# Performance work log

Hardware: AMD Instinct MI355X
Metric: run time of the kernel (lower is better)

## Reference

```python
import jax, jax.numpy as jnp
import numpy as np

D_MODEL = 1024
N_HEADS = 16
D_K = D_MODEL // N_HEADS
B, S = 2, 2048


def setup_inputs() -> dict:
    key = jax.random.key(0)
    ks = jax.random.split(key, 12)
    scale = 1.0 / np.sqrt(D_MODEL)
    inp = {
        "query": jax.random.normal(ks[0], (B, S, D_MODEL), jnp.float32),
        "key": jax.random.normal(ks[1], (B, S, D_MODEL), jnp.float32),
        "value": jax.random.normal(ks[2], (B, S, D_MODEL), jnp.float32),
        "mask": jnp.tril(jnp.ones((S, S), dtype=bool))[None, None],  # (1,1,S,S) causal
        "W_q": jax.random.normal(ks[3], (D_MODEL, D_MODEL), jnp.float32) * scale,
        "b_q": jnp.zeros((D_MODEL,), jnp.float32),
        "W_k": jax.random.normal(ks[4], (D_MODEL, D_MODEL), jnp.float32) * scale,
        "b_k": jnp.zeros((D_MODEL,), jnp.float32),
        "W_v": jax.random.normal(ks[5], (D_MODEL, D_MODEL), jnp.float32) * scale,
        "b_v": jnp.zeros((D_MODEL,), jnp.float32),
        "W_o": jax.random.normal(ks[6], (D_MODEL, D_MODEL), jnp.float32) * scale,
        "b_o": jnp.zeros((D_MODEL,), jnp.float32),
    }
    return inp


def reference(query, key, value, mask, W_q, b_q, W_k, b_k, W_v, b_v, W_o, b_o):
    b = query.shape[0]
    # Linear projections (torch Linear: x @ W.T + b), split into heads -> (b,h,s,d_k)
    def proj(x, W, bias):
        y = x @ W.T + bias
        return y.reshape(b, -1, N_HEADS, D_K).transpose(0, 2, 1, 3)

    q = proj(query, W_q, b_q)
    k = proj(key, W_k, b_k)
    v = proj(value, W_v, b_v)

    # scores: (b,h,sq,sk)
    scores = jnp.einsum("bhqd,bhkd->bhqk", q, k) / jnp.sqrt(jnp.float32(D_K)).astype(q.dtype)
    scores = jnp.where(mask, scores, jnp.finfo(scores.dtype).min)
    attn = jax.nn.softmax(scores, axis=-1)
    out = jnp.einsum("bhqk,bhkd->bhqd", attn, v)  # (b,h,sq,d_k)
    out = out.transpose(0, 2, 1, 3).reshape(b, -1, D_MODEL)
    return out @ W_o.T + b_o
```

## Files before the change

kernel.cpp:

```cpp
#include <hip/hip_runtime.h>
#include <hip/hip_bf16.h>
#include <stdint.h>

#define D_MODEL 1024
#define NH 16
#define DK 64
#define BB 2
#define SS 2048
#define MROWS (BB*SS)

typedef __attribute__((ext_vector_type(8))) short bf16x8;
typedef __attribute__((ext_vector_type(4))) float f32x4;

__device__ __forceinline__ short to_bf16(float f) {
  __hip_bfloat16 h = __float2bfloat16(f);
  union { __hip_bfloat16 b; short s; } u; u.b = h; return u.s;
}

__device__ __forceinline__ f32x4 mfma16(bf16x8 a, bf16x8 b, f32x4 c) {
  return __builtin_amdgcn_mfma_f32_16x16x32_bf16(a, b, c, 0, 0, 0);
}

__device__ __forceinline__ void gload_lds16(const void* g, void* l) {
  __builtin_amdgcn_global_load_lds(
      (const __attribute__((address_space(1))) unsigned int*)g,
      (__attribute__((address_space(3))) unsigned int*)l,
      16, 0, 0);
}

__global__ __launch_bounds__(256) void cvt3(const float* __restrict__ a,
                                            const float* __restrict__ b,
                                            const float* __restrict__ c,
                                            short* __restrict__ oa,
                                            short* __restrict__ ob,
                                            short* __restrict__ oc) {
  const int z = blockIdx.z;
  const float* x = z == 0 ? a : z == 1 ? b : c;
  short* y = z == 0 ? oa : z == 1 ? ob : oc;
  const int i = (blockIdx.x * 256 + threadIdx.x) * 4;
  const float4 v = *(const float4*)(x + i);
  short4 o;
  o.x = to_bf16(v.x); o.y = to_bf16(v.y); o.z = to_bf16(v.z); o.w = to_bf16(v.w);
  *(short4*)(y + i) = o;
}

__global__ __launch_bounds__(256) void cvt4(const float* __restrict__ a,
                                            const float* __restrict__ b,
                                            const float* __restrict__ c,
                                            const float* __restrict__ d,
                                            short* __restrict__ oa,
                                            short* __restrict__ ob,
                                            short* __restrict__ oc,
                                            short* __restrict__ od) {
  const int z = blockIdx.z;
  const float* x = z == 0 ? a : z == 1 ? b : z == 2 ? c : d;
  short* y = z == 0 ? oa : z == 1 ? ob : z == 2 ? oc : od;
  const int i = (blockIdx.x * 256 + threadIdx.x) * 4;
  const float4 v = *(const float4*)(x + i);
  short4 o;
  o.x = to_bf16(v.x); o.y = to_bf16(v.y); o.z = to_bf16(v.z); o.w = to_bf16(v.w);
  *(short4*)(y + i) = o;
}

__global__ __launch_bounds__(256) void gemm_qkv(const short* __restrict__ Xq,
                                                const short* __restrict__ Xk,
                                                const short* __restrict__ Xv,
                                                const short* __restrict__ Wq,
                                                const short* __restrict__ Wk,
                                                const short* __restrict__ Wv,
                                                const float* __restrict__ bq,
                                                const float* __restrict__ bk,
                                                const float* __restrict__ bv,
                                                short* __restrict__ Qh,
                                                short* __restrict__ Kh,
                                                short* __restrict__ VT) {
  constexpr int K = 1024;
  __shared__ short As[128 * 64];
  __shared__ short Bs[128 * 64];
  const int z = blockIdx.z;
  const short* A    = z == 0 ? Xq : z == 1 ? Xk : Xv;
  const short* Wt   = z == 0 ? Wq : z == 1 ? Wk : Wv;
  const float* bias = z == 0 ? bq : z == 1 ? bk : bv;

  const int tid = threadIdx.x;
  const int w = tid >> 6, lane = tid & 63;
  const int m0 = blockIdx.x * 128, n0 = blockIdx.y * 128;
  const int wm = w >> 1, wn = w & 1;
  const int fr = lane & 15, fg = lane >> 4;
  const int srow = tid >> 3, scol = (tid & 7) * 8;

  f32x4 acc[4][4] = {};

  for (int k0 = 0; k0 < K; k0 += 64) {
    __syncthreads();
#pragma unroll
    for (int i = 0; i < 4; ++i) {
      const int row = i * 32 + srow;
      gload_lds16(A  + (size_t)(m0 + row) * K + k0 + scol, As + row * 64 + scol);
      gload_lds16(Wt + (size_t)(n0 + row) * K + k0 + scol, Bs + row * 64 + scol);
    }
    asm volatile("s_waitcnt vmcnt(0)" ::: "memory");
    __syncthreads();

    bf16x8 af[4][2], bfr[4][2];
#pragma unroll
    for (int i = 0; i < 4; ++i)
#pragma unroll
      for (int hh = 0; hh < 2; ++hh) {
        af[i][hh]  = *(const bf16x8*)(As + (wm * 64 + i * 16 + fr) * 64 + hh * 32 + fg * 8);
        bfr[i][hh] = *(const bf16x8*)(Bs + (wn * 64 + i * 16 + fr) * 64 + hh * 32 + fg * 8);
      }
    __builtin_amdgcn_s_setprio(1);
#pragma unroll
    for (int mi = 0; mi < 4; ++mi)
#pragma unroll
      for (int ni = 0; ni < 4; ++ni) {
        acc[mi][ni] = mfma16(af[mi][0], bfr[ni][0], acc[mi][ni]);
        acc[mi][ni] = mfma16(af[mi][1], bfr[ni][1], acc[mi][ni]);
      }
    __builtin_amdgcn_s_setprio(0);
  }

  const float scale = (z == 0) ? 0.18033688011112042f : 1.0f;
#pragma unroll
  for (int mi = 0; mi < 4; ++mi)
#pragma unroll
    for (int ni = 0; ni < 4; ++ni) {
      const int col = n0 + wn * 64 + ni * 16 + fr;
      const float bval = bias[col];
      const int h = col >> 6, d = col & 63;
#pragma unroll
      for (int r = 0; r < 4; ++r) {
        const int row = m0 + wm * 64 + mi * 16 + fg * 4 + r;
        const float val = (acc[mi][ni][r] + bval) * scale;
        const int b = row >> 11, s = row & (SS - 1);
        if (z < 2) {
          short* dst = (z == 0) ? Qh : Kh;
          dst[((size_t)(b * NH + h) * SS + s) * DK + d] = to_bf16(val);
        } else {
          VT[((size_t)(b * NH + h) * DK + d) * SS + s] = to_bf16(val);
        }
      }
    }
}

__global__ __launch_bounds__(256) void gemm_out(const short* __restrict__ A,
                                                const short* __restrict__ Wt,
                                                const float* __restrict__ bias,
                                                float* __restrict__ Y) {
  constexpr int K = 1024;
  __shared__ short As[128 * 64];
  __shared__ short Bs[64 * 64];
  const int tid = threadIdx.x;
  const int w = tid >> 6, lane = tid & 63;
  const int m0 = blockIdx.x * 128, n0 = blockIdx.y * 64;
  const int wm = w >> 1, wn = w & 1;
  const int fr = lane & 15, fg = lane >> 4;
  const int srow = tid >> 3, scol = (tid & 7) * 8;

  f32x4 acc[4][2] = {};

  for (int k0 = 0; k0 < K; k0 += 64) {
    __syncthreads();
#pragma unroll
    for (int i = 0; i < 4; ++i) {
      const int row = i * 32 + srow;
      gload_lds16(A + (size_t)(m0 + row) * K + k0 + scol, As + row * 64 + scol);
    }
#pragma unroll
    for (int i = 0; i < 2; ++i) {
      const int row = i * 32 + srow;
      gload_lds16(Wt + (size_t)(n0 + row) * K + k0 + scol, Bs + row * 64 + scol);
    }
    asm volatile("s_waitcnt vmcnt(0)" ::: "memory");
    __syncthreads();

    bf16x8 af[4][2], bfr[2][2];
#pragma unroll
    for (int i = 0; i < 4; ++i)
#pragma unroll
      for (int hh = 0; hh < 2; ++hh)
        af[i][hh] = *(const bf16x8*)(As + (wm * 64 + i * 16 + fr) * 64 + hh * 32 + fg * 8);
#pragma unroll
    for (int i = 0; i < 2; ++i)
#pragma unroll
      for (int hh = 0; hh < 2; ++hh)
        bfr[i][hh] = *(const bf16x8*)(Bs + (wn * 32 + i * 16 + fr) * 64 + hh * 32 + fg * 8);
    __builtin_amdgcn_s_setprio(1);
#pragma unroll
    for (int mi = 0; mi < 4; ++mi)
#pragma unroll
      for (int ni = 0; ni < 2; ++ni) {
        acc[mi][ni] = mfma16(af[mi][0], bfr[ni][0], acc[mi][ni]);
        acc[mi][ni] = mfma16(af[mi][1], bfr[ni][1], acc[mi][ni]);
      }
    __builtin_amdgcn_s_setprio(0);
  }

#pragma unroll
  for (int mi = 0; mi < 4; ++mi)
#pragma unroll
    for (int ni = 0; ni < 2; ++ni) {
      const int col = n0 + wn * 32 + ni * 16 + fr;
      const float bval = bias[col];
#pragma unroll
      for (int r = 0; r < 4; ++r) {
        const int row = m0 + wm * 64 + mi * 16 + fg * 4 + r;
        Y[(size_t)row * D_MODEL + col] = acc[mi][ni][r] + bval;
      }
    }
}

__global__ __launch_bounds__(256, 2) void attn_kernel(const short* __restrict__ Qh,
                                                      const short* __restrict__ Kh,
                                                      const short* __restrict__ VT,
                                                      short* __restrict__ AO) {
  __shared__ short P_lds[4][2][16 * 64];
  const int tid = threadIdx.x, w = tid >> 6, lane = tid & 63;
  const int fr = lane & 15, fg = lane >> 4;
  const int kr = fg * 4;

  const int bid = blockIdx.x;
  const int lid = ((bid & 7) << 6) | (bid >> 3);
  const int bh = lid >> 4;
  const int xq = lid & 15;
  const int b = bh >> 4, h = bh & 15;

  const int strip = (w == 0) ? xq : (w == 1) ? (31 - xq) : (w == 2) ? (32 + xq) : (63 - xq);
  const int q0w = strip * 32;

  const short* Qp = Qh + (size_t)bh * SS * DK;
  const short* Kp = Kh + (size_t)bh * SS * DK;
  const short* Vp = VT + (size_t)bh * DK * SS;

  bf16x8 qf[2][2];
#pragma unroll
  for (int qt = 0; qt < 2; ++qt)
#pragma unroll
    for (int hh = 0; hh < 2; ++hh)
      qf[qt][hh] = *(const bf16x8*)(Qp + (size_t)(q0w + qt * 16 + fr) * DK + hh * 32 + fg * 8);

  const short onev = (fr == 0) ? (short)0x3F80 : (short)0;
  const bf16x8 af4 = {onev, onev, onev, onev, onev, onev, onev, onev};

  f32x4 o[5][2] = {};
  float m_run[2] = {-1e30f, -1e30f};

  const int nfull = q0w >> 6;
  const int swz = (fr & 7) << 4;

  bf16x8 kf[4][2];
#pragma unroll
  for (int kt = 0; kt < 4; ++kt)
#pragma unroll
    for (int hh = 0; hh < 2; ++hh)
      kf[kt][hh] = *(const bf16x8*)(Kp + (size_t)(kt * 16 + fr) * DK + hh * 32 + fg * 8);

  for (int ti = 0; ti <= nfull; ++ti) {
    const int k0 = ti * 64;
    const bool hasNext = ti < nfull;

    bf16x8 kn[4][2];
    if (hasNext) {
#pragma unroll
      for (int kt = 0; kt < 4; ++kt)
#pragma unroll
        for (int hh = 0; hh < 2; ++hh)
          kn[kt][hh] = *(const bf16x8*)(Kp + (size_t)(k0 + 64 + kt * 16 + fr) * DK + hh * 32 + fg * 8);
    }

    f32x4 st[4][2] = {};
    __builtin_amdgcn_s_setprio(1);
#pragma unroll
    for (int kt = 0; kt < 4; ++kt)
#pragma unroll
      for (int qt = 0; qt < 2; ++qt) {
        st[kt][qt] = mfma16(kf[kt][0], qf[qt][0], st[kt][qt]);
        st[kt][qt] = mfma16(kf[kt][1], qf[qt][1], st[kt][qt]);
      }
    __builtin_amdgcn_s_setprio(0);

    bf16x8 vf[2][4];
#pragma unroll
    for (int c = 0; c < 2; ++c)
#pragma unroll
      for (int t = 0; t < 4; ++t)
        vf[c][t] = *(const bf16x8*)(Vp + (size_t)(t * 16 + fr) * SS + k0 + c * 32 + fg * 8);

    if (ti == nfull) {
#pragma unroll
      for (int kt = 0; kt < 4; ++kt)
#pragma unroll
        for (int qt = 0; qt < 2; ++qt)
#pragma unroll
          for (int r = 0; r < 4; ++r)
            if (k0 + kt * 16 + kr + r > q0w + qt * 16 + fr) st[kt][qt][r] = -1e30f;
    }

    float pmax[2];
#pragma unroll
    for (int qt = 0; qt < 2; ++qt) {
      float mt = st[0][qt][0];
#pragma unroll
      for (int kt = 0; kt < 4; ++kt)
#pragma unroll
        for (int r = 0; r < 4; ++r) mt = fmaxf(mt, st[kt][qt][r]);
      mt = fmaxf(mt, __shfl_xor(mt, 16));
      mt = fmaxf(mt, __shfl_xor(mt, 32));
      pmax[qt] = mt;
    }

    const bool ok = (pmax[0] <= m_run[0] + 11.0f) && (pmax[1] <= m_run[1] + 11.0f);
    if (!__all(ok)) {
#pragma unroll
      for (int qt = 0; qt < 2; ++qt) {
        const float mn = fmaxf(m_run[qt], pmax[qt]);
        const float al = __builtin_amdgcn_exp2f(m_run[qt] - mn);
        m_run[qt] = mn;
#pragma unroll
        for (int t = 0; t < 5; ++t)
#pragma unroll
          for (int r = 0; r < 4; ++r) o[t][qt][r] *= al;
      }
    }

#pragma unroll
    for (int qt = 0; qt < 2; ++qt) {
      char* base = (char*)P_lds[w][qt];
#pragma unroll
      for (int kt = 0; kt < 4; ++kt) {
        short4 sv;
        sv.x = to_bf16(__builtin_amdgcn_exp2f(st[kt][qt][0] - m_run[qt]));
        sv.y = to_bf16(__builtin_amdgcn_exp2f(st[kt][qt][1] - m_run[qt]));
        sv.z = to_bf16(__builtin_amdgcn_exp2f(st[kt][qt][2] - m_run[qt]));
        sv.w = to_bf16(__builtin_amdgcn_exp2f(st[kt][qt][3] - m_run[qt]));
        *(short4*)(base + ((fr * 128 + kt * 32 + fg * 8) ^ swz)) = sv;
      }
    }
    asm volatile("s_waitcnt lgkmcnt(0)" ::: "memory");

    bf16x8 pf[2][2];
#pragma unroll
    for (int qt = 0; qt < 2; ++qt)
#pragma unroll
      for (int c = 0; c < 2; ++c)
        pf[qt][c] = *(const bf16x8*)((const char*)P_lds[w][qt] + ((fr * 128 + c * 64 + fg * 16) ^ swz));

    __builtin_amdgcn_s_setprio(1);
#pragma unroll
    for (int c = 0; c < 2; ++c)
#pragma unroll
      for (int qt = 0; qt < 2; ++qt) {
#pragma unroll
        for (int t = 0; t < 4; ++t)
          o[t][qt] = mfma16(vf[c][t], pf[qt][c], o[t][qt]);
        o[4][qt] = mfma16(af4, pf[qt][c], o[4][qt]);
      }
    __builtin_amdgcn_s_setprio(0);

    if (hasNext) {
#pragma unroll
      for (int kt = 0; kt < 4; ++kt)
#pragma unroll
        for (int hh = 0; hh < 2; ++hh) kf[kt][hh] = kn[kt][hh];
    }
  }

#pragma unroll
  for (int qt = 0; qt < 2; ++qt) {
    const float l = __shfl(o[4][qt][0], fr);
    const float inv = 1.0f / l;
    const int s = q0w + qt * 16 + fr;
#pragma unroll
    for (int t = 0; t < 4; ++t) {
      short4 ov = {to_bf16(o[t][qt][0] * inv), to_bf16(o[t][qt][1] * inv),
                   to_bf16(o[t][qt][2] * inv), to_bf16(o[t][qt][3] * inv)};
      *(short4*)(AO + (size_t)(b * SS + s) * D_MODEL + h * 64 + t * 16 + kr) = ov;
    }
  }
}

extern "C" void kernel_launch(void* const* d_in, const int* in_sizes, int n_in,
                              void* d_out, int out_size, void* d_ws, size_t ws_size,
                              hipStream_t stream) {
  const float* q  = (const float*)d_in[0];
  const float* k  = (const float*)d_in[1];
  const float* v  = (const float*)d_in[2];
  const float* Wq = (const float*)d_in[4];
  const float* bq = (const float*)d_in[5];
  const float* Wk = (const float*)d_in[6];
  const float* bk = (const float*)d_in[7];
  const float* Wv = (const float*)d_in[8];
  const float* bv = (const float*)d_in[9];
  const float* Wo = (const float*)d_in[10];
  const float* bo = (const float*)d_in[11];

  char* ws = (char*)d_ws;
  const size_t MB = 1u << 20;
  short* Xq = (short*)(ws + 0 * MB);
  short* Xk = (short*)(ws + 8 * MB);
  short* Xv = (short*)(ws + 16 * MB);
  short* Bq = (short*)(ws + 24 * MB);
  short* Bk = (short*)(ws + 26 * MB);
  short* Bv = (short*)(ws + 28 * MB);
  short* Bo = (short*)(ws + 30 * MB);
  short* Qh = (short*)(ws + 32 * MB);
  short* Kh = (short*)(ws + 40 * MB);
  short* VT = (short*)(ws + 48 * MB);
  short* AO = (short*)(ws + 56 * MB);

  cvt3<<<dim3(MROWS * D_MODEL / 1024, 1, 3), 256, 0, stream>>>(q, k, v, Xq, Xk, Xv);
  cvt4<<<dim3(D_MODEL * D_MODEL / 1024, 1, 4), 256, 0, stream>>>(Wq, Wk, Wv, Wo, Bq, Bk, Bv, Bo);

  gemm_qkv<<<dim3(MROWS / 128, D_MODEL / 128, 3), 256, 0, stream>>>(
      Xq, Xk, Xv, Bq, Bk, Bv, bq, bk, bv, Qh, Kh, VT);

  attn_kernel<<<dim3(512), 256, 0, stream>>>(Qh, Kh, VT, AO);

  gemm_out<<<dim3(MROWS / 128, D_MODEL / 64), 256, 0, stream>>>(AO, Bo, bo, (float*)d_out);
}
```

Before: 144.4 us.

## Split each attention query strip's KV range across two waves and merge partials

Each block now handles two query strips instead of four, and each strip's causal key range is split between two waves. The waves keep separate online-softmax state, exchange running max and partial outputs through shared memory, and merge them with rescaling before the final normalization. The grid doubles to 1024 blocks, which shortens the longest per-wave loop and raises parallelism. The cost is a block-wide sync, extra shared-memory traffic for the partial accumulators, and more LDS per block, which may limit occupancy.

```diff
diff --git a/kernel.cpp b/kernel.cpp
--- a/kernel.cpp
+++ b/kernel.cpp
@@ -216,17 +216,22 @@
                                                       const short* __restrict__ VT,
                                                       short* __restrict__ AO) {
   __shared__ short P_lds[4][2][16 * 64];
+  __shared__ float M_lds[2][2][16];
+  __shared__ f32x4 O_lds[2][5][2][64];
+
   const int tid = threadIdx.x, w = tid >> 6, lane = tid & 63;
   const int fr = lane & 15, fg = lane >> 4;
   const int kr = fg * 4;
 
   const int bid = blockIdx.x;
-  const int lid = ((bid & 7) << 6) | (bid >> 3);
-  const int bh = lid >> 4;
-  const int xq = lid & 15;
+  const int lid = ((bid & 7) << 7) | (bid >> 3);
+  const int bh = lid >> 5;
+  const int pidx = lid & 31;
   const int b = bh >> 4, h = bh & 15;
 
-  const int strip = (w == 0) ? xq : (w == 1) ? (31 - xq) : (w == 2) ? (32 + xq) : (63 - xq);
+  const int ss = w >> 1;
+  const int half = w & 1;
+  const int strip = (ss == 0) ? pidx : (63 - pidx);
   const int q0w = strip * 32;
 
   const short* Qp = Qh + (size_t)bh * SS * DK;
@@ -246,19 +251,24 @@
   f32x4 o[5][2] = {};
   float m_run[2] = {-1e30f, -1e30f};
 
-  const int nfull = q0w >> 6;
+  const int T = (q0w >> 6) + 1;
+  const int tbeg = half ? (T >> 1) : 0;
+  const int tend = half ? T : (T >> 1);
+  const int Tm1 = T - 1;
   const int swz = (fr & 7) << 4;
 
   bf16x8 kf[4][2];
-#pragma unroll
-  for (int kt = 0; kt < 4; ++kt)
-#pragma unroll
-    for (int hh = 0; hh < 2; ++hh)
-      kf[kt][hh] = *(const bf16x8*)(Kp + (size_t)(kt * 16 + fr) * DK + hh * 32 + fg * 8);
-
-  for (int ti = 0; ti <= nfull; ++ti) {
+  if (tbeg < tend) {
+#pragma unroll
+    for (int kt = 0; kt < 4; ++kt)
+#pragma unroll
+      for (int hh = 0; hh < 2; ++hh)
+        kf[kt][hh] = *(const bf16x8*)(Kp + (size_t)(tbeg * 64 + kt * 16 + fr) * DK + hh * 32 + fg * 8);
+  }
+
+  for (int ti = tbeg; ti < tend; ++ti) {
     const int k0 = ti * 64;
-    const bool hasNext = ti < nfull;
+    const bool hasNext = (ti + 1) < tend;
 
     bf16x8 kn[4][2];
     if (hasNext) {
@@ -287,7 +297,7 @@
       for (int t = 0; t < 4; ++t)
         vf[c][t] = *(const bf16x8*)(Vp + (size_t)(t * 16 + fr) * SS + k0 + c * 32 + fg * 8);
 
-    if (ti == nfull) {
+    if (ti == Tm1) {
 #pragma unroll
       for (int kt = 0; kt < 4; ++kt)
 #pragma unroll
@@ -366,16 +376,41 @@
     }
   }
 
-#pragma unroll
-  for (int qt = 0; qt < 2; ++qt) {
-    const float l = __shfl(o[4][qt][0], fr);
-    const float inv = 1.0f / l;
-    const int s = q0w + qt * 16 + fr;
-#pragma unroll
-    for (int t = 0; t < 4; ++t) {
-      short4 ov = {to_bf16(o[t][qt][0] * inv), to_bf16(o[t][qt][1] * inv),
-                   to_bf16(o[t][qt][2] * inv), to_bf16(o[t][qt][3] * inv)};
-      *(short4*)(AO + (size_t)(b * SS + s) * D_MODEL + h * 64 + t * 16 + kr) = ov;
+  if (half == 1) {
+    if (fg == 0) {
+      M_lds[ss][0][fr] = m_run[0];
+      M_lds[ss][1][fr] = m_run[1];
+    }
+#pragma unroll
+    for (int t = 0; t < 5; ++t)
+#pragma unroll
+      for (int qt = 0; qt < 2; ++qt)
+        O_lds[ss][t][qt][lane] = o[t][qt];
+  }
+  __syncthreads();
+  if (half == 0) {
+#pragma unroll
+    for (int qt = 0; qt < 2; ++qt) {
+      const float mB = M_lds[ss][qt][fr];
+      const float mm = fmaxf(m_run[qt], mB);
+      const float aA = __builtin_amdgcn_exp2f(m_run[qt] - mm);
+      const float aB = __builtin_amdgcn_exp2f(mB - mm);
+#pragma unroll
+      for (int t = 0; t < 5; ++t)
+        o[t][qt] = o[t][qt] * aA + O_lds[ss][t][qt][lane] * aB;
+    }
+
+#pragma unroll
+    for (int qt = 0; qt < 2; ++qt) {
+      const float l = __shfl(o[4][qt][0], fr);
+      const float inv = 1.0f / l;
+      const int s = q0w + qt * 16 + fr;
+#pragma unroll
+      for (int t = 0; t < 4; ++t) {
+        short4 ov = {to_bf16(o[t][qt][0] * inv), to_bf16(o[t][qt][1] * inv),
+                     to_bf16(o[t][qt][2] * inv), to_bf16(o[t][qt][3] * inv)};
+        *(short4*)(AO + (size_t)(b * SS + s) * D_MODEL + h * 64 + t * 16 + kr) = ov;
+      }
     }
   }
 }
@@ -415,7 +450,7 @@
   gemm_qkv<<<dim3(MROWS / 128, D_MODEL / 128, 3), 256, 0, stream>>>(
       Xq, Xk, Xv, Bq, Bk, Bv, bq, bk, bv, Qh, Kh, VT);
 
-  attn_kernel<<<dim3(512), 256, 0, stream>>>(Qh, Kh, VT, AO);
+  attn_kernel<<<dim3(1024), 256, 0, stream>>>(Qh, Kh, VT, AO);
 
   gemm_out<<<dim3(MROWS / 128, D_MODEL / 64), 256, 0, stream>>>(AO, Bo, bo, (float*)d_out);
 }
```

After: 148.4 us. 2.7% more time.

## Share double-buffered K/V tiles in LDS across waves in attention kernel

Applied to the files above, without the earlier changes.

Restructures the attention kernel so each block handles one contiguous 64-row query tile. Each wave owns 16 query rows, and K/V tiles are staged cooperatively into swizzled, double-buffered LDS through global_load_lds. Before, every wave read K and V straight from global memory for its own 32-row strips. The grid doubles to 1024 blocks and launch bounds rise to 4 blocks per CU. The aim is to cut redundant global K/V traffic and raise occupancy, at the cost of a __syncthreads every tile and less per-wave work to hide latency.

```diff
diff --git a/kernel.cpp b/kernel.cpp
--- a/kernel.cpp
+++ b/kernel.cpp
@@ -211,172 +211,152 @@
     }
 }
 
-__global__ __launch_bounds__(256, 2) void attn_kernel(const short* __restrict__ Qh,
+__global__ __launch_bounds__(256, 4) void attn_kernel(const short* __restrict__ Qh,
                                                       const short* __restrict__ Kh,
                                                       const short* __restrict__ VT,
                                                       short* __restrict__ AO) {
-  __shared__ short P_lds[4][2][16 * 64];
+  __shared__ short Ks[2][64 * 64];
+  __shared__ short Vs[2][64 * 64];
+  __shared__ short P_lds[4][16 * 64];
+
   const int tid = threadIdx.x, w = tid >> 6, lane = tid & 63;
   const int fr = lane & 15, fg = lane >> 4;
   const int kr = fg * 4;
+  const int swz = (fr & 7) << 4;
 
   const int bid = blockIdx.x;
-  const int lid = ((bid & 7) << 6) | (bid >> 3);
-  const int bh = lid >> 4;
-  const int xq = lid & 15;
+  const int lid = ((bid & 7) << 7) | (bid >> 3);
+  const int bh = lid >> 5;
+  const int idx = lid & 31;
+  const int P = (idx & 1) ? (31 - (idx >> 1)) : (idx >> 1);
   const int b = bh >> 4, h = bh & 15;
-
-  const int strip = (w == 0) ? xq : (w == 1) ? (31 - xq) : (w == 2) ? (32 + xq) : (63 - xq);
-  const int q0w = strip * 32;
+  const int qw = P * 64 + w * 16;
 
   const short* Qp = Qh + (size_t)bh * SS * DK;
   const short* Kp = Kh + (size_t)bh * SS * DK;
   const short* Vp = VT + (size_t)bh * DK * SS;
 
-  bf16x8 qf[2][2];
-#pragma unroll
-  for (int qt = 0; qt < 2; ++qt)
-#pragma unroll
-    for (int hh = 0; hh < 2; ++hh)
-      qf[qt][hh] = *(const bf16x8*)(Qp + (size_t)(q0w + qt * 16 + fr) * DK + hh * 32 + fg * 8);
+  const int sc_c = tid & 7;
+  const int sc_r = tid >> 3;
+
+  bf16x8 qf[2];
+#pragma unroll
+  for (int hh = 0; hh < 2; ++hh)
+    qf[hh] = *(const bf16x8*)(Qp + (size_t)(qw + fr) * DK + hh * 32 + fg * 8);
 
   const short onev = (fr == 0) ? (short)0x3F80 : (short)0;
   const bf16x8 af4 = {onev, onev, onev, onev, onev, onev, onev, onev};
 
-  f32x4 o[5][2] = {};
-  float m_run[2] = {-1e30f, -1e30f};
-
-  const int nfull = q0w >> 6;
-  const int swz = (fr & 7) << 4;
-
-  bf16x8 kf[4][2];
-#pragma unroll
-  for (int kt = 0; kt < 4; ++kt)
-#pragma unroll
-    for (int hh = 0; hh < 2; ++hh)
-      kf[kt][hh] = *(const bf16x8*)(Kp + (size_t)(kt * 16 + fr) * DK + hh * 32 + fg * 8);
-
-  for (int ti = 0; ti <= nfull; ++ti) {
-    const int k0 = ti * 64;
-    const bool hasNext = ti < nfull;
-
-    bf16x8 kn[4][2];
-    if (hasNext) {
+  f32x4 o[5] = {};
+  float m_run = -1e30f;
+
+  const int T = P + 1;
+
+#define STAGE_KV(buf, t0)                                                     \
+  do {                                                                        \
+    const int kk0 = (t0) * 64;                                                \
+    _Pragma("unroll") for (int p = 0; p < 2; ++p) {                           \
+      const int row = p * 32 + sc_r;                                          \
+      const int sc = sc_c ^ (row & 7);                                        \
+      gload_lds16(Kp + (size_t)(kk0 + row) * DK + sc * 8,                     \
+                  &Ks[buf][row * 64 + sc_c * 8]);                             \
+      gload_lds16(Vp + (size_t)row * SS + kk0 + sc * 8,                       \
+                  &Vs[buf][row * 64 + sc_c * 8]);                             \
+    }                                                                         \
+  } while (0)
+
+  STAGE_KV(0, 0);
+  asm volatile("s_waitcnt vmcnt(0)" ::: "memory");
+  __syncthreads();
+
+  for (int ti = 0; ti < T; ++ti) {
+    const int cur = ti & 1;
+    if (ti + 1 < T) STAGE_KV(cur ^ 1, ti + 1);
+
+    const char* KsB = (const char*)Ks[cur];
+    const char* VsB = (const char*)Vs[cur];
+
+    f32x4 st[4];
+    __builtin_amdgcn_s_setprio(1);
+#pragma unroll
+    for (int kt = 0; kt < 4; ++kt) {
+      const bf16x8 k0f = *(const bf16x8*)(KsB + (kt * 16 + fr) * 128 + ((fg * 16) ^ swz));
+      const bf16x8 k1f = *(const bf16x8*)(KsB + (kt * 16 + fr) * 128 + ((64 + fg * 16) ^ swz));
+      f32x4 z = {};
+      z = mfma16(k0f, qf[0], z);
+      z = mfma16(k1f, qf[1], z);
+      st[kt] = z;
+    }
+    __builtin_amdgcn_s_setprio(0);
+
+    if (ti == T - 1) {
 #pragma unroll
       for (int kt = 0; kt < 4; ++kt)
 #pragma unroll
-        for (int hh = 0; hh < 2; ++hh)
-          kn[kt][hh] = *(const bf16x8*)(Kp + (size_t)(k0 + 64 + kt * 16 + fr) * DK + hh * 32 + fg * 8);
-    }
-
-    f32x4 st[4][2] = {};
-    __builtin_amdgcn_s_setprio(1);
+        for (int r = 0; r < 4; ++r)
+          if (kt * 16 + kr + r > w * 16 + fr) st[kt][r] = -1e30f;
+    }
+
+    float pmax = st[0][0];
 #pragma unroll
     for (int kt = 0; kt < 4; ++kt)
 #pragma unroll
-      for (int qt = 0; qt < 2; ++qt) {
-        st[kt][qt] = mfma16(kf[kt][0], qf[qt][0], st[kt][qt]);
-        st[kt][qt] = mfma16(kf[kt][1], qf[qt][1], st[kt][qt]);
-      }
-    __builtin_amdgcn_s_setprio(0);
-
-    bf16x8 vf[2][4];
-#pragma unroll
-    for (int c = 0; c < 2; ++c)
-#pragma unroll
-      for (int t = 0; t < 4; ++t)
-        vf[c][t] = *(const bf16x8*)(Vp + (size_t)(t * 16 + fr) * SS + k0 + c * 32 + fg * 8);
-
-    if (ti == nfull) {
-#pragma unroll
-      for (int kt = 0; kt < 4; ++kt)
-#pragma unroll
-        for (int qt = 0; qt < 2; ++qt)
-#pragma unroll
-          for (int r = 0; r < 4; ++r)
-            if (k0 + kt * 16 + kr + r > q0w + qt * 16 + fr) st[kt][qt][r] = -1e30f;
-    }
-
-    float pmax[2];
-#pragma unroll
-    for (int qt = 0; qt < 2; ++qt) {
-      float mt = st[0][qt][0];
-#pragma unroll
-      for (int kt = 0; kt < 4; ++kt)
-#pragma unroll
-        for (int r = 0; r < 4; ++r) mt = fmaxf(mt, st[kt][qt][r]);
-      mt = fmaxf(mt, __shfl_xor(mt, 16));
-      mt = fmaxf(mt, __shfl_xor(mt, 32));
-      pmax[qt] = mt;
-    }
-
-    const bool ok = (pmax[0] <= m_run[0] + 11.0f) && (pmax[1] <= m_run[1] + 11.0f);
-    if (!__all(ok)) {
-#pragma unroll
-      for (int qt = 0; qt < 2; ++qt) {
-        const float mn = fmaxf(m_run[qt], pmax[qt]);
-        const float al = __builtin_amdgcn_exp2f(m_run[qt] - mn);
-        m_run[qt] = mn;
-#pragma unroll
-        for (int t = 0; t < 5; ++t)
-#pragma unroll
-          for (int r = 0; r < 4; ++r) o[t][qt][r] *= al;
-      }
-    }
-
-#pragma unroll
-    for (int qt = 0; qt < 2; ++qt) {
-      char* base = (char*)P_lds[w][qt];
+      for (int r = 0; r < 4; ++r) pmax = fmaxf(pmax, st[kt][r]);
+    pmax = fmaxf(pmax, __shfl_xor(pmax, 16));
+    pmax = fmaxf(pmax, __shfl_xor(pmax, 32));
+
+    if (!__all(pmax <= m_run + 11.0f)) {
+      const float mn = fmaxf(m_run, pmax);
+      const float al = __builtin_amdgcn_exp2f(m_run - mn);
+      m_run = mn;
+#pragma unroll
+      for (int t = 0; t < 5; ++t)
+#pragma unroll
+        for (int r = 0; r < 4; ++r) o[t][r] *= al;
+    }
+
+    {
+      char* base = (char*)P_lds[w];
 #pragma unroll
       for (int kt = 0; kt < 4; ++kt) {
         short4 sv;
-        sv.x = to_bf16(__builtin_amdgcn_exp2f(st[kt][qt][0] - m_run[qt]));
-        sv.y = to_bf16(__builtin_amdgcn_exp2f(st[kt][qt][1] - m_run[qt]));
-        sv.z = to_bf16(__builtin_amdgcn_exp2f(st[kt][qt][2] - m_run[qt]));
-        sv.w = to_bf16(__builtin_amdgcn_exp2f(st[kt][qt][3] - m_run[qt]));
+        sv.x = to_bf16(__builtin_amdgcn_exp2f(st[kt][0] - m_run));
+        sv.y = to_bf16(__builtin_amdgcn_exp2f(st[kt][1] - m_run));
+        sv.z = to_bf16(__builtin_amdgcn_exp2f(st[kt][2] - m_run));
+        sv.w = to_bf16(__builtin_amdgcn_exp2f(st[kt][3] - m_run));
         *(short4*)(base + ((fr * 128 + kt * 32 + fg * 8) ^ swz)) = sv;
       }
     }
     asm volatile("s_waitcnt lgkmcnt(0)" ::: "memory");
 
-    bf16x8 pf[2][2];
-#pragma unroll
-    for (int qt = 0; qt < 2; ++qt)
-#pragma unroll
-      for (int c = 0; c < 2; ++c)
-        pf[qt][c] = *(const bf16x8*)((const char*)P_lds[w][qt] + ((fr * 128 + c * 64 + fg * 16) ^ swz));
-
     __builtin_amdgcn_s_setprio(1);
 #pragma unroll
-    for (int c = 0; c < 2; ++c)
-#pragma unroll
-      for (int qt = 0; qt < 2; ++qt) {
-#pragma unroll
-        for (int t = 0; t < 4; ++t)
-          o[t][qt] = mfma16(vf[c][t], pf[qt][c], o[t][qt]);
-        o[4][qt] = mfma16(af4, pf[qt][c], o[4][qt]);
-      }
+    for (int c = 0; c < 2; ++c) {
+      const bf16x8 pf = *(const bf16x8*)((const char*)P_lds[w] +
+                                         ((fr * 128 + c * 64 + fg * 16) ^ swz));
+#pragma unroll
+      for (int t = 0; t < 4; ++t) {
+        const bf16x8 vfb = *(const bf16x8*)(VsB + (t * 16 + fr) * 128 +
+                                            ((c * 64 + fg * 16) ^ swz));
+        o[t] = mfma16(vfb, pf, o[t]);
+      }
+      o[4] = mfma16(af4, pf, o[4]);
+    }
     __builtin_amdgcn_s_setprio(0);
 
-    if (hasNext) {
-#pragma unroll
-      for (int kt = 0; kt < 4; ++kt)
-#pragma unroll
-        for (int hh = 0; hh < 2; ++hh) kf[kt][hh] = kn[kt][hh];
-    }
+    asm volatile("s_waitcnt vmcnt(0)" ::: "memory");
+    __syncthreads();
   }
-
-#pragma unroll
-  for (int qt = 0; qt < 2; ++qt) {
-    const float l = __shfl(o[4][qt][0], fr);
-    const float inv = 1.0f / l;
-    const int s = q0w + qt * 16 + fr;
-#pragma unroll
-    for (int t = 0; t < 4; ++t) {
-      short4 ov = {to_bf16(o[t][qt][0] * inv), to_bf16(o[t][qt][1] * inv),
-                   to_bf16(o[t][qt][2] * inv), to_bf16(o[t][qt][3] * inv)};
-      *(short4*)(AO + (size_t)(b * SS + s) * D_MODEL + h * 64 + t * 16 + kr) = ov;
-    }
+#undef STAGE_KV
+
+  const float l = __shfl(o[4][0], fr);
+  const float inv = 1.0f / l;
+  const int s = qw + fr;
+#pragma unroll
+  for (int t = 0; t < 4; ++t) {
+    short4 ov = {to_bf16(o[t][0] * inv), to_bf16(o[t][1] * inv),
+                 to_bf16(o[t][2] * inv), to_bf16(o[t][3] * inv)};
+    *(short4*)(AO + (size_t)(b * SS + s) * D_MODEL + h * 64 + t * 16 + kr) = ov;
   }
 }
 
@@ -415,7 +395,7 @@
   gemm_qkv<<<dim3(MROWS / 128, D_MODEL / 128, 3), 256, 0, stream>>>(
       Xq, Xk, Xv, Bq, Bk, Bv, bq, bk, bv, Qh, Kh, VT);
 
-  attn_kernel<<<dim3(512), 256, 0, stream>>>(Qh, Kh, VT, AO);
+  attn_kernel<<<dim3(1024), 256, 0, stream>>>(Qh, Kh, VT, AO);
 
   gemm_out<<<dim3(MROWS / 128, D_MODEL / 64), 256, 0, stream>>>(AO, Bo, bo, (float*)d_out);
 }
```

New measurement: 133.9 us. 7.3% less time.
